# Performance work log

Hardware: AMD Instinct MI355X
Metric: run time of the kernel (lower is better)

Reference implementation:

```python
import jax, jax.numpy as jnp
import numpy as np

EPS = 1e-5
B, N, E, D, ED, F = 4096, 22, 42, 128, 32, 2048

def _ln(x, g, b):
    m = jnp.mean(x, axis=-1, keepdims=True)
    v = jnp.var(x, axis=-1, keepdims=True)
    return (x - m) * jax.lax.rsqrt(v + EPS) * g + b

def setup_inputs() -> dict:
    key = jax.random.key(0)
    ks = jax.random.split(key, 24)
    def rn(k, shp, scale=0.05):
        return jax.random.normal(k, shp, dtype=jnp.float32) * scale
    return {
        "node_features": jax.random.normal(ks[0], (B, N, D), dtype=jnp.float32),
        "edge_attr": jax.random.normal(ks[1], (B, E, ED), dtype=jnp.float32),
        "aggregation_matrix": jax.random.uniform(ks[2], (N, E), dtype=jnp.float32),
        "source_indices": jax.random.randint(ks[3], (E,), 0, N, dtype=jnp.int32),
        "target_indices": jax.random.randint(ks[4], (E,), 0, N, dtype=jnp.int32),
        # edge MLP: Linear(2D+ED -> 4*ED), ReLU, Linear(4*ED -> ED)
        "ew1": rn(ks[5], (2 * D + ED, 4 * ED)), "eb1": jnp.zeros((4 * ED,), jnp.float32),
        "ew2": rn(ks[6], (4 * ED, ED)), "eb2": jnp.zeros((ED,), jnp.float32),
        # message projection ED -> D
        "pw": rn(ks[7], (ED, D)), "pb": jnp.zeros((D,), jnp.float32),
        # gated update gates: 2D -> D each
        "rw": rn(ks[8], (2 * D, D)), "rb": jnp.zeros((D,), jnp.float32),
        "uw": rn(ks[9], (2 * D, D)), "ub": jnp.zeros((D,), jnp.float32),
        "cw": rn(ks[10], (2 * D, D)), "cb": jnp.zeros((D,), jnp.float32),
        # layernorms
        "g1": jnp.ones((D,), jnp.float32), "be1": jnp.zeros((D,), jnp.float32),
        "g2": jnp.ones((D,), jnp.float32), "be2": jnp.zeros((D,), jnp.float32),
        # FFN D -> F -> D
        "fw1": rn(ks[11], (D, F)), "fb1": jnp.zeros((F,), jnp.float32),
        "fw2": rn(ks[12], (F, D)), "fb2": jnp.zeros((D,), jnp.float32),
    }

def reference(node_features, edge_attr, aggregation_matrix, source_indices, target_indices,
              ew1, eb1, ew2, eb2, pw, pb, rw, rb, uw, ub, cw, cb,
              g1, be1, g2, be2, fw1, fb1, fw2, fb2):
    normed = _ln(node_features, g1, be1)                      # [B,N,D]
    src = jnp.take(normed, source_indices, axis=1)            # [B,E,D]
    tgt = jnp.take(normed, target_indices, axis=1)            # [B,E,D]
    combined = jnp.concatenate([src, tgt, edge_attr], axis=-1)  # [B,E,2D+ED]
    h = jax.nn.relu(combined @ ew1 + eb1)
    edge_messages = h @ ew2 + eb2                             # [B,E,ED]
    aggregated = jnp.einsum('ne,bed->bnd', aggregation_matrix, edge_messages)  # [B,N,ED]
    projected = aggregated @ pw + pb                          # [B,N,D]
    # GRU-style gated update
    nm = jnp.concatenate([normed, projected], axis=-1)
    reset = jax.nn.sigmoid(nm @ rw + rb)
    update = jax.nn.sigmoid(nm @ uw + ub)
    rc = jnp.concatenate([reset * normed, projected], axis=-1)
    cand = jnp.tanh(rc @ cw + cb)
    x = node_features + (1.0 - update) * normed + update * cand
    # norm + FFN (dropout = identity in eval mode)
    n2 = _ln(x, g2, be2)
    ff = jax.nn.gelu(n2 @ fw1 + fb1, approximate=False) @ fw2 + fb2
    return (x + ff, edge_messages)
```

## Files before the change

### kernel.cpp

```cpp
#include <hip/hip_runtime.h>
#include <math.h>

#define NB 4096
#define NN 22
#define NE 42
#define DD 128
#define ED2 32
#define HH 128
#define FF 2048
#define HCHUNKS 32

typedef float f32x4 __attribute__((ext_vector_type(4)));
typedef short s16x8 __attribute__((ext_vector_type(8)));

__device__ __forceinline__ float sigmoidf_(float x){ return 1.f/(1.f+__expf(-x)); }

__device__ __forceinline__ unsigned short f2bf(float f){
  unsigned u = __float_as_uint(f);
  u += 0x7fffu + ((u >> 16) & 1u);
  return (unsigned short)(u >> 16);
}
__device__ __forceinline__ float bf2f(unsigned short h){
  return __uint_as_float(((unsigned)h) << 16);
}
__device__ __forceinline__ float gelu_f(float x){
  float x2 = x*x;
  float inner = fmaf(0.044715f*x2, x, x);
  float p = __builtin_amdgcn_exp2f(2.3022085f*inner);
  float t = __builtin_amdgcn_rcpf(p + 1.f);
  return fmaf(-x, t, x);
}

__device__ __forceinline__ void gld16(const void* g, void* l){
  __builtin_amdgcn_global_load_lds((__attribute__((address_space(1))) void*)g,
                                   (__attribute__((address_space(3))) void*)l, 16, 0, 0);
}
template<int BYTES, int NW>
__device__ __forceinline__ void stage_lds(void* lbase, const void* gbase, int wave, int lane){
  const int per = BYTES / NW;
  const int ni  = per / 1024;
  const char* g = (const char*)gbase + wave*per + lane*16;
  char* l = (char*)lbase + wave*per;
  #pragma unroll
  for (int i=0;i<ni;i++) gld16(g + i*1024, l + i*1024);
}

#define S_VMCNT(N) { asm volatile("s_waitcnt vmcnt(" #N ")" ::: "memory"); __builtin_amdgcn_sched_barrier(0); }
#define S_LGKM0()  { asm volatile("s_waitcnt lgkmcnt(0)" ::: "memory"); __builtin_amdgcn_sched_barrier(0); }
#define RAW_BAR()  { asm volatile("s_waitcnt lgkmcnt(0)" ::: "memory"); __builtin_amdgcn_sched_barrier(0); __builtin_amdgcn_s_barrier(); __builtin_amdgcn_sched_barrier(0); }

__device__ __forceinline__ int fragidx128(int c, int k){
  return ((c>>4)*4 + (k>>5))*512 + (((k>>3)&3)*16 + (c&15))*8 + (k&7);
}
__device__ __forceinline__ int fragidx64(int c, int k){
  return ((c>>4)*2 + (k>>5))*512 + (((k>>3)&3)*16 + (c&15))*8 + (k&7);
}

__global__ __launch_bounds__(256) void wconv_kernel(
    const float* __restrict__ fw1, const float* __restrict__ fw2,
    const float* __restrict__ ew1, const float* __restrict__ ew2,
    const float* __restrict__ rw, const float* __restrict__ uw, const float* __restrict__ cw,
    const float* __restrict__ pw, const float* __restrict__ aggm,
    unsigned short* __restrict__ w1t, unsigned short* __restrict__ w2b,
    unsigned short* __restrict__ ewc, unsigned short* __restrict__ ew2c,
    unsigned short* __restrict__ gw,
    unsigned short* __restrict__ tailf, unsigned short* __restrict__ pwf,
    unsigned short* __restrict__ aggmf)
{
  const int idx = blockIdx.x*256 + threadIdx.x;
  {
    const int k = idx >> 11, j = idx & 2047;
    w1t[(j>>7)*16384 + fragidx128(j&127, k)] = f2bf(fw1[idx]);
  }
  {
    const int kg = idx >> 7, c = idx & 127;
    w2b[(kg>>6)*8192 + fragidx64(c, kg&63)] = f2bf(fw2[idx]);
  }
  if (idx < 32768) {
    const int c2 = idx >> 7, k = idx & 127;
    const int part = c2 >> 7, c = c2 & 127;
    const float v = ew1[(part*128 + k)*DD + c];
    ewc[part*16384 + ((k>>5)*8 + (c>>4))*512 + (((k>>3)&3)*16 + (c&15))*8 + (k&7)] = f2bf(v);
  }
  if (idx < 4096) {
    const int m = idx & 31, k = idx >> 5;
    ew2c[fragidx128(m, k)] = f2bf(ew2[k*ED2 + m]);
  }
  if (idx < 4096) {
    const int k = idx >> 7, c = idx & 127;
    const int u = (c>>4)*512 + ((k>>3)*16 + (c&15))*8 + (k&7);
    tailf[u] = f2bf(ew1[(256 + k)*DD + c]);
    pwf[u]  = f2bf(pw[k*DD + c]);
  }
  if (idx < 2048) {
    const int n = idx >> 6, e = idx & 63;
    const float v = (n < NN && e < NE) ? aggm[n*NE + e] : 0.f;
    aggmf[(n>>4)*1024 + (e>>5)*512 + (((e>>3)&3)*16 + (n&15))*8 + (e&7)] = f2bf(v);
  }
  if (idx < 98304) {
    const int gate = idx >> 15;
    const int rem  = idx & 32767;
    const int half = rem >> 14, c = (rem >> 7) & 127, k = rem & 127;
    const float* wsrc = (gate==0) ? rw : ((gate==1) ? uw : cw);
    const float v = wsrc[(half*128 + k)*128 + c];
    gw[gate*32768 + half*16384 + (k>>6)*8192 + fragidx64(c, k&63)] = f2bf(v);
  }
}

__global__ __launch_bounds__(256) void edge_mfma_kernel(
    const float* __restrict__ nf, const float* __restrict__ ea,
    const int* __restrict__ src, const int* __restrict__ tgt,
    const float* __restrict__ eb1, const float* __restrict__ eb2,
    const float* __restrict__ pb,
    const unsigned short* __restrict__ ewc2,
    const unsigned short* __restrict__ ew2c,
    const unsigned short* __restrict__ tailf,
    const unsigned short* __restrict__ pwf,
    const unsigned short* __restrict__ aggmf,
    const float* __restrict__ g1, const float* __restrict__ be1,
    float* __restrict__ out_em, float* __restrict__ out_x)
{
  const int b = blockIdx.x, t = threadIdx.x, lane = t & 63, wave = t >> 6;

  __shared__ __align__(16) char s_lds[77184];
  unsigned short* s_w0  = (unsigned short*)(s_lds);
  unsigned short* s_w1  = (unsigned short*)(s_lds + 16384);
  unsigned short* s_emf = (unsigned short*)(s_lds + 16384);
  unsigned short* s_ew2 = (unsigned short*)(s_lds + 32768);
  unsigned short* s_agm = (unsigned short*)(s_lds + 40960);
  unsigned short* s_pw  = (unsigned short*)(s_lds + 45056);
  char*           s_a   = s_lds + 53248;
  char*           s_h   = s_lds + 61440;
  unsigned short* s_eaf = (unsigned short*)(s_lds + 73728);
  unsigned short* s_agf = (unsigned short*)(s_lds + 73728);
  int*            s_srcA= (int*)(s_lds + 76800);
  int*            s_tgtA= (int*)(s_lds + 76992);

  stage_lds<16384,4>(s_w0, ewc2, wave, lane);
  stage_lds<8192,4>(s_ew2, ew2c, wave, lane);
  stage_lds<4096,4>(s_agm, aggmf, wave, lane);
  stage_lds<8192,4>(s_pw, pwf, wave, lane);

  for (int r = wave; r < NN; r += 4) {
    const float* row = nf + ((size_t)b*NN + r)*DD;
    float x0 = row[lane], x1 = row[lane+64];
    float s = x0+x1, ss = x0*x0+x1*x1;
    #pragma unroll
    for (int off=32; off>=1; off>>=1) { s += __shfl_xor(s,off); ss += __shfl_xor(ss,off); }
    float m = s*(1.f/128.f);
    float inv = rsqrtf(ss*(1.f/128.f)-m*m + 1e-5f);
    float n0 = (x0-m)*inv*g1[lane]+be1[lane];
    float n1 = (x1-m)*inv*g1[lane+64]+be1[lane+64];
    char* base = s_a + r*256;
    const int sw = (r&7)<<4;
    *(unsigned short*)(base + ((lane*2)      ^ sw)) = f2bf(n0);
    *(unsigned short*)(base + (((lane+64)*2) ^ sw)) = f2bf(n1);
  }
  for (int i=t; i<640; i+=256) ((float*)(s_a + NN*256))[i] = 0.f;

  if (t < 48) { s_srcA[t] = (t < NE) ? src[t] : NN; s_tgtA[t] = (t < NE) ? tgt[t] : NN; }

  if (t < 168) {
    const int e = t >> 2, kb = t & 3;
    const float* p = ea + ((size_t)b*NE + e)*ED2 + kb*8;
    const float4 v0 = *(const float4*)p;
    const float4 v1 = *(const float4*)(p+4);
    unsigned long long lo = (unsigned long long)f2bf(v0.x) | ((unsigned long long)f2bf(v0.y)<<16)
                          | ((unsigned long long)f2bf(v0.z)<<32) | ((unsigned long long)f2bf(v0.w)<<48);
    unsigned long long hi = (unsigned long long)f2bf(v1.x) | ((unsigned long long)f2bf(v1.y)<<16)
                          | ((unsigned long long)f2bf(v1.z)<<32) | ((unsigned long long)f2bf(v1.w)<<48);
    unsigned long long* dst = (unsigned long long*)(s_eaf + (e>>4)*512 + (kb*16 + (e&15))*8);
    dst[0] = lo; dst[1] = hi;
  } else if (t < 192) {
    const int idx = t - 168;
    const int kb = idx / 6, er = 10 + idx % 6;
    unsigned long long* dst = (unsigned long long*)(s_eaf + 2*512 + (kb*16 + er)*8);
    dst[0] = 0ull; dst[1] = 0ull;
  }

  __syncthreads();

  const int frow = lane & 15;
  const int gsel = (lane >> 4) << 4;
  const int nt0 = wave*2;

  int rowS[3], rowT[3];
  #pragma unroll
  for (int mt=0; mt<3; ++mt){
    rowS[mt] = s_srcA[mt*16 + frow];
    rowT[mt] = s_tgtA[mt*16 + frow];
  }

  f32x4 hacc[3][2];
  #pragma unroll
  for (int mt=0; mt<3; ++mt){
    hacc[mt][0] = (f32x4){0.f,0.f,0.f,0.f};
    hacc[mt][1] = (f32x4){0.f,0.f,0.f,0.f};
  }

  #define HROUND(WCP, ROWS, KOFF) { \
    const unsigned short* wc_ = (WCP); \
    _Pragma("unroll") \
    for (int mt=0; mt<3; ++mt){ \
      const int r_ = (ROWS)[mt]; \
      const int sw_ = (r_&7)<<4; \
      const s16x8 a0 = *(const s16x8*)(s_a + r_*256 + (((KOFF) + gsel)^sw_)); \
      const s16x8 a1 = *(const s16x8*)(s_a + r_*256 + (((KOFF) + 64 + gsel)^sw_)); \
      _Pragma("unroll") \
      for (int ntl=0; ntl<2; ++ntl){ \
        const s16x8 b0 = *(const s16x8*)(wc_ + (    nt0+ntl)*512 + lane*8); \
        const s16x8 b1 = *(const s16x8*)(wc_ + (8 + nt0+ntl)*512 + lane*8); \
        hacc[mt][ntl] = __builtin_amdgcn_mfma_f32_16x16x32_bf16(a0, b0, hacc[mt][ntl], 0,0,0); \
        hacc[mt][ntl] = __builtin_amdgcn_mfma_f32_16x16x32_bf16(a1, b1, hacc[mt][ntl], 0,0,0); \
      } \
    } }

  stage_lds<16384,4>(s_w1, ewc2 + 8192, wave, lane);
  HROUND(s_w0, rowS, 0);
  S_VMCNT(0);
  RAW_BAR();
  stage_lds<16384,4>(s_w0, ewc2 + 16384, wave, lane);
  HROUND(s_w1, rowS, 128);
  S_VMCNT(0);
  RAW_BAR();
  stage_lds<16384,4>(s_w1, ewc2 + 24576, wave, lane);
  HROUND(s_w0, rowT, 0);
  S_VMCNT(0);
  RAW_BAR();
  stage_lds<8192,4>(s_w0, tailf, wave, lane);
  HROUND(s_w1, rowT, 128);
  S_VMCNT(0);
  RAW_BAR();
  #undef HROUND

  { uint4 z; z.x=0u; z.y=0u; z.z=0u; z.w=0u; *(uint4*)((char*)s_emf + t*16) = z; }
  #pragma unroll
  for (int mt=0; mt<3; ++mt){
    const s16x8 ae = *(const s16x8*)(s_eaf + mt*512 + lane*8);
    #pragma unroll
    for (int ntl=0; ntl<2; ++ntl){
      const s16x8 bt = *(const s16x8*)(s_w0 + (nt0+ntl)*512 + lane*8);
      hacc[mt][ntl] = __builtin_amdgcn_mfma_f32_16x16x32_bf16(ae, bt, hacc[mt][ntl], 0,0,0);
    }
  }
  #pragma unroll
  for (int mt=0; mt<3; ++mt){
    #pragma unroll
    for (int ntl=0; ntl<2; ++ntl){
      const int c = (nt0+ntl)*16 + frow;
      const float e1 = eb1[c];
      #pragma unroll
      for (int reg=0; reg<4; ++reg){
        const int e = mt*16 + (lane>>4)*4 + reg;
        const float v = fmaxf(hacc[mt][ntl][reg] + e1, 0.f);
        *(unsigned short*)(s_h + e*256 + ((c*2) ^ ((e&7)<<4))) = (e < NE) ? f2bf(v) : (unsigned short)0;
      }
    }
  }
  RAW_BAR();

  for (int id = wave; id < 6; id += 4) {
    const int mt = id >> 1, ntn = id & 1;
    f32x4 acc2 = (f32x4){0.f,0.f,0.f,0.f};
    #pragma unroll
    for (int ks=0; ks<4; ++ks){
      const s16x8 av = *(const s16x8*)(s_h + (mt*16 + frow)*256 + ((ks*64 + gsel) ^ ((frow&7)<<4)));
      const s16x8 bv = *(const s16x8*)(s_ew2 + (ntn*4+ks)*512 + lane*8);
      acc2 = __builtin_amdgcn_mfma_f32_16x16x32_bf16(av, bv, acc2, 0,0,0);
    }
    const int mc = ntn*16 + frow;
    const float bias = eb2[mc];
    #pragma unroll
    for (int reg=0; reg<4; ++reg){
      const int e = mt*16 + (lane>>4)*4 + reg;
      if (e < NE) {
        const float v = acc2[reg] + bias;
        out_em[((size_t)b*NE + e)*ED2 + mc] = v;
        s_emf[(mc>>4)*1024 + (e>>5)*512 + (((e>>3)&3)*16 + (mc&15))*8 + (e&7)] = f2bf(v);
      }
    }
  }
  RAW_BAR();

  {
    const int mt = wave >> 1, ntn = wave & 1;
    f32x4 acc3 = (f32x4){0.f,0.f,0.f,0.f};
    #pragma unroll
    for (int ks=0; ks<2; ++ks){
      const s16x8 av = *(const s16x8*)(s_agm + (mt*2+ks)*512 + lane*8);
      const s16x8 bv = *(const s16x8*)(s_emf + (ntn*2+ks)*512 + lane*8);
      acc3 = __builtin_amdgcn_mfma_f32_16x16x32_bf16(av, bv, acc3, 0,0,0);
    }
    const int mc = ntn*16 + frow;
    #pragma unroll
    for (int reg=0; reg<4; ++reg){
      const int n = mt*16 + (lane>>4)*4 + reg;
      s_agf[(n>>4)*512 + (((mc>>3)&3)*16 + (n&15))*8 + (mc&7)] = f2bf(acc3[reg]);
    }
  }
  RAW_BAR();

  #pragma unroll
  for (int ii=0; ii<4; ++ii){
    const int id = wave + ii*4;
    const int mt = id >> 3, nt = id & 7;
    const s16x8 av = *(const s16x8*)(s_agf + mt*512 + lane*8);
    const s16x8 bv = *(const s16x8*)(s_pw + nt*512 + lane*8);
    f32x4 a4 = __builtin_amdgcn_mfma_f32_16x16x32_bf16(av, bv, (f32x4){0.f,0.f,0.f,0.f}, 0,0,0);
    const int c = nt*16 + frow;
    const float pbv = pb[c];
    #pragma unroll
    for (int reg=0; reg<4; ++reg){
      const int n = mt*16 + (lane>>4)*4 + reg;
      *(unsigned short*)(s_a + n*256 + ((c*2) ^ ((n&7)<<4))) = f2bf(a4[reg] + pbv);
    }
  }
  RAW_BAR();

  for (int o=t; o<NN*16; o+=256){
    const int n = o>>4, cell = o&15;
    const int k0 = (cell>>2)*32 + (cell&3)*8;
    const uint4 v = *(const uint4*)(s_a + n*256 + ((k0*2) ^ ((n&7)<<4)));
    *(uint4*)((char*)out_x + (((size_t)b*NN + n)*512) + cell*16) = v;
  }
}

__global__ __launch_bounds__(256) void gate_mfma_kernel(
    const float* __restrict__ nf,
    const float* __restrict__ rb, const float* __restrict__ ub, const float* __restrict__ cbv,
    const float* __restrict__ g1, const float* __restrict__ be1,
    const unsigned short* __restrict__ gw,
    float* __restrict__ out_x)
{
  const int t=threadIdx.x, lane=t&63, wave=t>>6;
  const size_t row0 = (size_t)blockIdx.x * 64;
  const int wrow = wave*16;

  __shared__ __align__(16) unsigned short s_nb[8192];
  __shared__ __align__(16) unsigned short s_pb[8192];
  __shared__ __align__(16) unsigned short s_w[2][8192];
  __shared__ float s_mean[64], s_inv[64];

  const char* gwb = (const char*)gw;

  stage_lds<16384,4>(s_w[0], gwb, wave, lane);

  for (int i=t; i<1024; i+=256){
    const int r = i>>4, cell = i&15;
    ((uint4*)s_pb)[((r>>4)*4 + (cell>>2))*64 + (cell&3)*16 + (r&15)] =
      *((const uint4*)(out_x + (row0+r)*DD) + cell);
  }

  for (int r16=0; r16<16; ++r16){
    const int row = wrow + r16;
    const float* xr = nf + (row0+row)*DD;
    float x0=xr[lane], x1=xr[lane+64];
    float s=x0+x1, ss=x0*x0+x1*x1;
    #pragma unroll
    for (int off=32; off>=1; off>>=1){ s+=__shfl_xor(s,off); ss+=__shfl_xor(ss,off); }
    float m=s*(1.f/128.f);
    float inv=rsqrtf(ss*(1.f/128.f)-m*m+1e-5f);
    if (lane==0){ s_mean[row]=m; s_inv[row]=inv; }
    float n0=(x0-m)*inv*g1[lane]+be1[lane];
    float n1=(x1-m)*inv*g1[lane+64]+be1[lane+64];
    const int mt = row>>4, fr = row&15;
    const int ks = lane>>5, g = (lane>>3)&3, j = lane&7;
    s_nb[(mt*4+ks)*512   + (g*16+fr)*8 + j] = f2bf(n0);
    s_nb[(mt*4+ks+2)*512 + (g*16+fr)*8 + j] = f2bf(n1);
  }
  __syncthreads();

  s16x8 aN[4], aP[4];
  #pragma unroll
  for (int kk=0; kk<4; ++kk){
    aN[kk] = *(const s16x8*)(s_nb + (wave*4+kk)*512 + lane*8);
    aP[kk] = *(const s16x8*)(s_pb + (wave*4+kk)*512 + lane*8);
  }

  f32x4 accR[8], accU[8], accC[8];
  #pragma unroll
  for (int nt=0; nt<8; ++nt){
    const int col = nt*16 + (lane&15);
    accR[nt] = (f32x4){rb[col],rb[col],rb[col],rb[col]};
    accU[nt] = (f32x4){ub[col],ub[col],ub[col],ub[col]};
    accC[nt] = (f32x4){cbv[col],cbv[col],cbv[col],cbv[col]};
  }

  #define GSTAGE(S, NEXT, ACC, A0, A1) { \
    if (NEXT) stage_lds<16384,4>(s_w[((S)+1)&1], gwb + ((S)+1)*16384, wave, lane); \
    unsigned short* sb = s_w[(S)&1]; \
    _Pragma("unroll") for (int nt=0;nt<8;++nt){ \
      const s16x8 b0 = *(const s16x8*)(sb + (nt*2+0)*512 + lane*8); \
      ACC[nt] = __builtin_amdgcn_mfma_f32_16x16x32_bf16(A0, b0, ACC[nt], 0,0,0); \
      const s16x8 b1 = *(const s16x8*)(sb + (nt*2+1)*512 + lane*8); \
      ACC[nt] = __builtin_amdgcn_mfma_f32_16x16x32_bf16(A1, b1, ACC[nt], 0,0,0); } \
    S_VMCNT(0); \
    RAW_BAR(); }

  GSTAGE(0, 1, accR, aN[0], aN[1]);
  GSTAGE(1, 1, accR, aN[2], aN[3]);
  GSTAGE(2, 1, accR, aP[0], aP[1]);
  GSTAGE(3, 1, accR, aP[2], aP[3]);

  #pragma unroll
  for (int nt=0; nt<8; ++nt){
    #pragma unroll
    for (int reg=0; reg<4; ++reg){
      const float r_ = sigmoidf_(accR[nt][reg]);
      const int frA = (lane>>4)*4 + reg;
      const int ks = nt>>1, g = ((nt&1)<<1) | ((lane&15)>>3), j = lane&7;
      unsigned short* p = s_nb + (wave*4+ks)*512 + (g*16+frA)*8 + j;
      *p = f2bf(r_ * bf2f(*p));
    }
  }
  s16x8 aRC[4];
  #pragma unroll
  for (int kk=0; kk<4; ++kk)
    aRC[kk] = *(const s16x8*)(s_nb + (wave*4+kk)*512 + lane*8);

  GSTAGE(4, 1, accU, aN[0], aN[1]);
  GSTAGE(5, 1, accU, aN[2], aN[3]);
  GSTAGE(6, 1, accU, aP[0], aP[1]);
  GSTAGE(7, 1, accU, aP[2], aP[3]);
  GSTAGE(8, 1, accC, aRC[0], aRC[1]);
  GSTAGE(9, 1, accC, aRC[2], aRC[3]);
  GSTAGE(10, 1, accC, aP[0], aP[1]);
  GSTAGE(11, 0, accC, aP[2], aP[3]);
  #undef GSTAGE

  #pragma unroll
  for (int nt=0; nt<8; ++nt){
    const int col = nt*16 + (lane&15);
    const float gg = g1[col], bb = be1[col];
    #pragma unroll
    for (int reg=0; reg<4; ++reg){
      const int rowl = wrow + (lane>>4)*4 + reg;
      const size_t grow = row0 + rowl;
      const float u_ = sigmoidf_(accU[nt][reg]);
      const float cand = tanhf(accC[nt][reg]);
      const float nfv = nf[grow*DD + col];
      const float nv = (nfv - s_mean[rowl])*s_inv[rowl]*gg + bb;
      out_x[grow*DD + col] = nfv + (1.f-u_)*nv + u_*cand;
    }
  }
}

__global__ __launch_bounds__(512) void ffn_mfma_kernel(
    float* __restrict__ out_x,
    const float* __restrict__ g2, const float* __restrict__ be2,
    const float* __restrict__ fb1, const float* __restrict__ fb2,
    const unsigned short* __restrict__ w1t,
    const unsigned short* __restrict__ w2b)
{
  const int t = threadIdx.x, lane = t & 63, wave = t >> 6;
  const size_t row0 = (size_t)blockIdx.x * 128;
  const int wrow = wave * 16;
  const int rg = wave >> 1, cg = wave & 1;

  __shared__ __align__(16) unsigned short s_buf[2][16384];
  __shared__ __align__(16) unsigned short s_hid[8192];

  stage_lds<16384,8>(s_buf[0],        w1t, wave, lane);
  stage_lds<16384,8>(s_buf[0] + 8192, w2b, wave, lane);

  for (int r16 = 0; r16 < 16; ++r16) {
    const int row = wrow + r16;
    const float* xr = out_x + (row0+row)*DD;
    float x0 = xr[lane], x1 = xr[lane+64];
    float s = x0+x1, ss = x0*x0+x1*x1;
    #pragma unroll
    for (int off=32; off>=1; off>>=1){ s+=__shfl_xor(s,off); ss+=__shfl_xor(ss,off); }
    float m = s*(1.f/128.f);
    float inv = rsqrtf(ss*(1.f/128.f)-m*m+1e-5f);
    float n0 = (x0-m)*inv*g2[lane]+be2[lane];
    float n1 = (x1-m)*inv*g2[lane+64]+be2[lane+64];
    const int fr = row&15;
    const int ks = lane>>5, g = (lane>>3)&3, j = lane&7;
    unsigned short* dst = s_buf[1] + (wave>>2)*8192;
    const int wv = wave & 3;
    dst[(wv*4+ks)*512   + (g*16+fr)*8 + j] = f2bf(n0);
    dst[(wv*4+ks+2)*512 + (g*16+fr)*8 + j] = f2bf(n1);
  }
  __syncthreads();

  const int frow = lane & 15;
  const int q = lane >> 4;

  s16x8 aN[2][4];
  #pragma unroll
  for (int mt=0; mt<2; ++mt){
    const int m = rg*2 + mt;
    const unsigned short* srcb = s_buf[1] + (m>>2)*8192;
    #pragma unroll
    for (int ks=0; ks<4; ++ks)
      aN[mt][ks] = *(const s16x8*)(srcb + ((m&3)*4+ks)*512 + lane*8);
  }
  RAW_BAR();

  const int hb = (rg*4 + cg)*512 + (((q>>1)*16 + frow)*8) + (q&1)*4;

  f32x4 accO[2][4];
  #pragma unroll
  for (int mt=0; mt<2; ++mt)
    #pragma unroll
    for (int nt=0; nt<4; ++nt)
      accO[mt][nt] = (f32x4){0.f,0.f,0.f,0.f};

  for (int hc = 0; hc < HCHUNKS; ++hc) {
    const unsigned short* cur = s_buf[hc & 1];
    unsigned short* nxt = s_buf[(hc + 1) & 1];
    if (hc < HCHUNKS-1) {
      stage_lds<16384,8>(nxt,        w1t + (hc+1)*8192, wave, lane);
      stage_lds<16384,8>(nxt + 8192, w2b + (hc+1)*8192, wave, lane);
    }

    f32x4 acc1[2][2];
    #pragma unroll
    for (int nt=0; nt<2; ++nt){
      const float4 bv = *(const float4*)(fb1 + hc*64 + cg*32 + nt*16 + (q<<2));
      acc1[0][nt] = (f32x4){bv.x, bv.y, bv.z, bv.w};
      acc1[1][nt] = acc1[0][nt];
    }
    #pragma unroll
    for (int nt=0; nt<2; ++nt){
      #pragma unroll
      for (int ks=0; ks<4; ++ks){
        const s16x8 ww = *(const s16x8*)(cur + ((cg*2+nt)*4+ks)*512 + lane*8);
        acc1[0][nt] = __builtin_amdgcn_mfma_f32_16x16x32_bf16(ww, aN[0][ks], acc1[0][nt], 0,0,0);
        acc1[1][nt] = __builtin_amdgcn_mfma_f32_16x16x32_bf16(ww, aN[1][ks], acc1[1][nt], 0,0,0);
      }
    }
    #pragma unroll
    for (int mt=0; mt<2; ++mt){
      #pragma unroll
      for (int nt=0; nt<2; ++nt){
        const float e0 = gelu_f(acc1[mt][nt][0]);
        const float e1 = gelu_f(acc1[mt][nt][1]);
        const float e2 = gelu_f(acc1[mt][nt][2]);
        const float e3 = gelu_f(acc1[mt][nt][3]);
        unsigned plo, phi;
        asm("v_cvt_pk_bf16_f32 %0, %1, %2" : "=v"(plo) : "v"(e0), "v"(e1));
        asm("v_cvt_pk_bf16_f32 %0, %1, %2" : "=v"(phi) : "v"(e2), "v"(e3));
        uint2 pk; pk.x = plo; pk.y = phi;
        *(uint2*)((char*)s_hid + (hb + mt*1024 + nt*256)*2) = pk;
      }
    }
    RAW_BAR();

    s16x8 aH[2][2];
    #pragma unroll
    for (int mt=0; mt<2; ++mt)
      #pragma unroll
      for (int ks=0; ks<2; ++ks)
        aH[mt][ks] = *(const s16x8*)(s_hid + ((rg*2+mt)*2+ks)*512 + lane*8);
    #pragma unroll
    for (int nt=0; nt<4; ++nt){
      #pragma unroll
      for (int ks=0; ks<2; ++ks){
        const s16x8 bb = *(const s16x8*)(cur + 8192 + ((cg*4+nt)*2+ks)*512 + lane*8);
        accO[0][nt] = __builtin_amdgcn_mfma_f32_16x16x32_bf16(aH[0][ks], bb, accO[0][nt], 0,0,0);
        accO[1][nt] = __builtin_amdgcn_mfma_f32_16x16x32_bf16(aH[1][ks], bb, accO[1][nt], 0,0,0);
      }
    }
    S_VMCNT(0);
    RAW_BAR();
  }

  #pragma unroll
  for (int mt=0; mt<2; ++mt){
    #pragma unroll
    for (int nt=0; nt<4; ++nt){
      const int colg = cg*64 + nt*16 + frow;
      const float bias = fb2[colg];
      #pragma unroll
      for (int reg=0; reg<4; ++reg){
        const size_t row = row0 + rg*32 + mt*16 + q*4 + reg;
        const float xo = out_x[row*DD + colg];
        out_x[row*DD + colg] = xo + bias + accO[mt][nt][reg];
      }
    }
  }
}

extern "C" void kernel_launch(void* const* d_in, const int* in_sizes, int n_in,
                              void* d_out, int out_size, void* d_ws, size_t ws_size,
                              hipStream_t stream) {
  const float* nf  = (const float*)d_in[0];
  const float* ea  = (const float*)d_in[1];
  const float* agg = (const float*)d_in[2];
  const int*   src = (const int*)d_in[3];
  const int*   tgt = (const int*)d_in[4];
  const float* ew1 = (const float*)d_in[5];
  const float* eb1 = (const float*)d_in[6];
  const float* ew2 = (const float*)d_in[7];
  const float* eb2 = (const float*)d_in[8];
  const float* pw  = (const float*)d_in[9];
  const float* pb  = (const float*)d_in[10];
  const float* rw  = (const float*)d_in[11];
  const float* rb  = (const float*)d_in[12];
  const float* uw  = (const float*)d_in[13];
  const float* ub  = (const float*)d_in[14];
  const float* cw  = (const float*)d_in[15];
  const float* cbv = (const float*)d_in[16];
  const float* g1  = (const float*)d_in[17];
  const float* be1 = (const float*)d_in[18];
  const float* g2  = (const float*)d_in[19];
  const float* be2 = (const float*)d_in[20];
  const float* fw1 = (const float*)d_in[21];
  const float* fb1 = (const float*)d_in[22];
  const float* fw2 = (const float*)d_in[23];
  const float* fb2 = (const float*)d_in[24];

  float* out_x  = (float*)d_out;
  float* out_em = (float*)d_out + (size_t)NB*NN*DD;

  unsigned short* w1t  = (unsigned short*)d_ws;
  unsigned short* w2b  = w1t + (size_t)FF*DD;
  unsigned short* ewc  = w2b + (size_t)FF*DD;
  unsigned short* ew2c = ewc + (size_t)256*128;
  unsigned short* gw   = ew2c + (size_t)32*128;
  unsigned short* tailf= gw + (size_t)3*32768;
  unsigned short* pwf  = tailf + 4096;
  unsigned short* aggmf= pwf + 4096;

  hipLaunchKernelGGL(wconv_kernel, dim3(1024), dim3(256), 0, stream,
                     fw1, fw2, ew1, ew2, rw, uw, cw, pw, agg,
                     w1t, w2b, ewc, ew2c, gw, tailf, pwf, aggmf);
  hipLaunchKernelGGL(edge_mfma_kernel, dim3(NB), dim3(256), 0, stream,
                     nf, ea, src, tgt, eb1, eb2, pb, ewc, ew2c, tailf, pwf, aggmf,
                     g1, be1, out_em, out_x);
  hipLaunchKernelGGL(gate_mfma_kernel, dim3(NB*NN/64), dim3(256), 0, stream,
                     nf, rb, ub, cbv, g1, be1, gw, out_x);
  hipLaunchKernelGGL(ffn_mfma_kernel, dim3(NB*NN/128), dim3(512), 0, stream,
                     out_x, g2, be2, fb1, fb2, w1t, w2b);
}
```

Measured before the change: 324.5 us.

## Process two batch elements per edge-kernel block to share staged weights

The edge kernel now runs 512 threads per block, with two groups of four waves each handling a different batch element. The bf16 edge-MLP weights, ew2, aggregation matrix and projection weights staged in LDS are shared between the two, so each staged weight serves twice as much work and the grid is halved. Per-batch scratch buffers (normalized rows, hidden activations, edge attrs, messages) are duplicated, which raises LDS use from about 77 KB to about 100 KB and may reduce how many blocks fit on a CU.

```diff
diff --git a/kernel.cpp b/kernel.cpp
--- a/kernel.cpp
+++ b/kernel.cpp
@@ -107,7 +107,7 @@
   }
 }
 
-__global__ __launch_bounds__(256) void edge_mfma_kernel(
+__global__ __launch_bounds__(512) void edge_mfma_kernel(
     const float* __restrict__ nf, const float* __restrict__ ea,
     const int* __restrict__ src, const int* __restrict__ tgt,
     const float* __restrict__ eb1, const float* __restrict__ eb2,
@@ -120,28 +120,32 @@
     const float* __restrict__ g1, const float* __restrict__ be1,
     float* __restrict__ out_em, float* __restrict__ out_x)
 {
-  const int b = blockIdx.x, t = threadIdx.x, lane = t & 63, wave = t >> 6;
-
-  __shared__ __align__(16) char s_lds[77184];
+  const int t = threadIdx.x, lane = t & 63, wave = t >> 6;
+  const int wv = wave & 3;
+  const int bb = wave >> 2;
+  const int b  = blockIdx.x*2 + bb;
+  const int th = t & 255;
+
+  __shared__ __align__(16) char s_lds[100736];
   unsigned short* s_w0  = (unsigned short*)(s_lds);
   unsigned short* s_w1  = (unsigned short*)(s_lds + 16384);
-  unsigned short* s_emf = (unsigned short*)(s_lds + 16384);
+  unsigned short* s_emf = (unsigned short*)(s_lds + 16384 + bb*4096);
   unsigned short* s_ew2 = (unsigned short*)(s_lds + 32768);
   unsigned short* s_agm = (unsigned short*)(s_lds + 40960);
   unsigned short* s_pw  = (unsigned short*)(s_lds + 45056);
-  char*           s_a   = s_lds + 53248;
-  char*           s_h   = s_lds + 61440;
-  unsigned short* s_eaf = (unsigned short*)(s_lds + 73728);
-  unsigned short* s_agf = (unsigned short*)(s_lds + 73728);
-  int*            s_srcA= (int*)(s_lds + 76800);
-  int*            s_tgtA= (int*)(s_lds + 76992);
-
-  stage_lds<16384,4>(s_w0, ewc2, wave, lane);
-  stage_lds<8192,4>(s_ew2, ew2c, wave, lane);
-  stage_lds<4096,4>(s_agm, aggmf, wave, lane);
-  stage_lds<8192,4>(s_pw, pwf, wave, lane);
-
-  for (int r = wave; r < NN; r += 4) {
+  char*           s_a   = s_lds + 53248 + bb*8192;
+  char*           s_h   = s_lds + 69632 + bb*12288;
+  unsigned short* s_eaf = (unsigned short*)(s_lds + 94208 + bb*3072);
+  unsigned short* s_agf = s_eaf;
+  int*            s_srcA= (int*)(s_lds + 100352);
+  int*            s_tgtA= (int*)(s_lds + 100544);
+
+  stage_lds<16384,8>(s_w0, ewc2, wave, lane);
+  stage_lds<8192,8>(s_ew2, ew2c, wave, lane);
+  if (wave < 4) stage_lds<4096,4>(s_agm, aggmf, wave, lane);
+  stage_lds<8192,8>(s_pw, pwf, wave, lane);
+
+  for (int r = wv; r < NN; r += 4) {
     const float* row = nf + ((size_t)b*NN + r)*DD;
     float x0 = row[lane], x1 = row[lane+64];
     float s = x0+x1, ss = x0*x0+x1*x1;
@@ -156,12 +160,12 @@
     *(unsigned short*)(base + ((lane*2)      ^ sw)) = f2bf(n0);
     *(unsigned short*)(base + (((lane+64)*2) ^ sw)) = f2bf(n1);
   }
-  for (int i=t; i<640; i+=256) ((float*)(s_a + NN*256))[i] = 0.f;
+  for (int i=th; i<640; i+=256) ((float*)(s_a + NN*256))[i] = 0.f;
 
   if (t < 48) { s_srcA[t] = (t < NE) ? src[t] : NN; s_tgtA[t] = (t < NE) ? tgt[t] : NN; }
 
-  if (t < 168) {
-    const int e = t >> 2, kb = t & 3;
+  if (th < 168) {
+    const int e = th >> 2, kb = th & 3;
     const float* p = ea + ((size_t)b*NE + e)*ED2 + kb*8;
     const float4 v0 = *(const float4*)p;
     const float4 v1 = *(const float4*)(p+4);
@@ -171,8 +175,8 @@
                           | ((unsigned long long)f2bf(v1.z)<<32) | ((unsigned long long)f2bf(v1.w)<<48);
     unsigned long long* dst = (unsigned long long*)(s_eaf + (e>>4)*512 + (kb*16 + (e&15))*8);
     dst[0] = lo; dst[1] = hi;
-  } else if (t < 192) {
-    const int idx = t - 168;
+  } else if (th < 192) {
+    const int idx = th - 168;
     const int kb = idx / 6, er = 10 + idx % 6;
     unsigned long long* dst = (unsigned long long*)(s_eaf + 2*512 + (kb*16 + er)*8);
     dst[0] = 0ull; dst[1] = 0ull;
@@ -182,7 +186,7 @@
 
   const int frow = lane & 15;
   const int gsel = (lane >> 4) << 4;
-  const int nt0 = wave*2;
+  const int nt0 = wv*2;
 
   int rowS[3], rowT[3];
   #pragma unroll
@@ -215,25 +219,25 @@
       } \
     } }
 
-  stage_lds<16384,4>(s_w1, ewc2 + 8192, wave, lane);
+  stage_lds<16384,8>(s_w1, ewc2 + 8192, wave, lane);
   HROUND(s_w0, rowS, 0);
   S_VMCNT(0);
   RAW_BAR();
-  stage_lds<16384,4>(s_w0, ewc2 + 16384, wave, lane);
+  stage_lds<16384,8>(s_w0, ewc2 + 16384, wave, lane);
   HROUND(s_w1, rowS, 128);
   S_VMCNT(0);
   RAW_BAR();
-  stage_lds<16384,4>(s_w1, ewc2 + 24576, wave, lane);
+  stage_lds<16384,8>(s_w1, ewc2 + 24576, wave, lane);
   HROUND(s_w0, rowT, 0);
   S_VMCNT(0);
   RAW_BAR();
-  stage_lds<8192,4>(s_w0, tailf, wave, lane);
+  stage_lds<8192,8>(s_w0, tailf, wave, lane);
   HROUND(s_w1, rowT, 128);
   S_VMCNT(0);
   RAW_BAR();
   #undef HROUND
 
-  { uint4 z; z.x=0u; z.y=0u; z.z=0u; z.w=0u; *(uint4*)((char*)s_emf + t*16) = z; }
+  { uint4 z; z.x=0u; z.y=0u; z.z=0u; z.w=0u; *(uint4*)(s_lds + 16384 + t*16) = z; }
   #pragma unroll
   for (int mt=0; mt<3; ++mt){
     const s16x8 ae = *(const s16x8*)(s_eaf + mt*512 + lane*8);
@@ -259,7 +263,7 @@
   }
   RAW_BAR();
 
-  for (int id = wave; id < 6; id += 4) {
+  for (int id = wv; id < 6; id += 4) {
     const int mt = id >> 1, ntn = id & 1;
     f32x4 acc2 = (f32x4){0.f,0.f,0.f,0.f};
     #pragma unroll
@@ -283,7 +287,7 @@
   RAW_BAR();
 
   {
-    const int mt = wave >> 1, ntn = wave & 1;
+    const int mt = wv >> 1, ntn = wv & 1;
     f32x4 acc3 = (f32x4){0.f,0.f,0.f,0.f};
     #pragma unroll
     for (int ks=0; ks<2; ++ks){
@@ -302,7 +306,7 @@
 
   #pragma unroll
   for (int ii=0; ii<4; ++ii){
-    const int id = wave + ii*4;
+    const int id = wv + ii*4;
     const int mt = id >> 3, nt = id & 7;
     const s16x8 av = *(const s16x8*)(s_agf + mt*512 + lane*8);
     const s16x8 bv = *(const s16x8*)(s_pw + nt*512 + lane*8);
@@ -317,7 +321,7 @@
   }
   RAW_BAR();
 
-  for (int o=t; o<NN*16; o+=256){
+  for (int o=th; o<NN*16; o+=256){
     const int n = o>>4, cell = o&15;
     const int k0 = (cell>>2)*32 + (cell&3)*8;
     const uint4 v = *(const uint4*)(s_a + n*256 + ((k0*2) ^ ((n&7)<<4)));
@@ -626,7 +630,7 @@
   hipLaunchKernelGGL(wconv_kernel, dim3(1024), dim3(256), 0, stream,
                      fw1, fw2, ew1, ew2, rw, uw, cw, pw, agg,
                      w1t, w2b, ewc, ew2c, gw, tailf, pwf, aggmf);
-  hipLaunchKernelGGL(edge_mfma_kernel, dim3(NB), dim3(256), 0, stream,
+  hipLaunchKernelGGL(edge_mfma_kernel, dim3(NB/2), dim3(512), 0, stream,
                      nf, ea, src, tgt, eb1, eb2, pb, ewc, ew2c, tailf, pwf, aggmf,
                      g1, be1, out_em, out_x);
   hipLaunchKernelGGL(gate_mfma_kernel, dim3(NB*NN/64), dim3(256), 0, stream,
```

After: 325.2 us. About the same (+0.2%).
